# Kernel optimization log

Measured on AMD Instinct MI355X. Metric: run time of the kernel, lower is better.

## Reference

```python
import jax, jax.numpy as jnp
import numpy as np

B, T, C, H = 8, 1024, 768, 12
D = C // H  # head_dim = 64


def setup_inputs() -> dict:
    key = jax.random.key(0)
    ks = jax.random.split(key, 6)
    s = 1.0 / np.sqrt(C)
    x = jax.random.normal(ks[0], (B, T, C), dtype=jnp.float32)
    Wq = jax.random.normal(ks[1], (C, C), dtype=jnp.float32) * s
    Wk = jax.random.normal(ks[2], (C, C), dtype=jnp.float32) * s
    Wv = jax.random.normal(ks[3], (C, C), dtype=jnp.float32) * s
    Wo = jax.random.normal(ks[4], (C, C), dtype=jnp.float32) * s
    bq = jnp.zeros((C,), jnp.float32)
    bk = jnp.zeros((C,), jnp.float32)
    bv = jnp.zeros((C,), jnp.float32)
    bo = jnp.zeros((C,), jnp.float32)
    # causal mask, broadcastable to [B, H, T, T]
    mask = jnp.tril(jnp.ones((T, T), dtype=bool))[None, None, :, :]
    return {"x": x, "mask": mask, "Wq": Wq, "bq": bq, "Wk": Wk, "bk": bk,
            "Wv": Wv, "bv": bv, "Wo": Wo, "bo": bo}


def reference(x, mask, Wq, bq, Wk, bk, Wv, bv, Wo, bo):
    # QKV projections: [B,T,C] @ [C,C] -> [B,T,C]
    q = x @ Wq + bq
    k = x @ Wk + bk
    v = x @ Wv + bv
    # split heads -> [B,H,T,D]
    q = q.reshape(B, T, H, D).transpose(0, 2, 1, 3)
    k = k.reshape(B, T, H, D).transpose(0, 2, 1, 3)
    v = v.reshape(B, T, H, D).transpose(0, 2, 1, 3)
    scale = 1.0 / jnp.sqrt(jnp.float32(D))
    scores = jnp.einsum('bhtd,bhsd->bhts', q, k) * scale  # [B,H,T,T]
    scores = jnp.where(mask, scores, jnp.float32(-1e9))
    attn = jax.nn.softmax(scores, axis=-1)
    out = jnp.einsum('bhts,bhsd->bhtd', attn, v)  # [B,H,T,D]
    out = out.transpose(0, 2, 1, 3).reshape(B, T, C)
    return out @ Wo + bo
```

## Files before the change

### kernel.cpp

```cpp
#include <hip/hip_runtime.h>

#define B 8
#define T 1024
#define C 768
#define H 12
#define D 64
#define M (B * T)

typedef unsigned short u16;
typedef unsigned int u32;
typedef __attribute__((ext_vector_type(8))) short bf16x8;
typedef __attribute__((ext_vector_type(4))) float f32x4;

__device__ __forceinline__ u16 f2bf(float f) {
  union { float f; u32 u; } c; c.f = f;
  u32 r = c.u + 0x7FFF + ((c.u >> 16) & 1);
  return (u16)(r >> 16);
}

__device__ __forceinline__ void gload16(const void* g, void* l) {
  __builtin_amdgcn_global_load_lds(
      (const __attribute__((address_space(1))) void*)g,
      (__attribute__((address_space(3))) void*)l, 16, 0, 0);
}

__device__ __forceinline__ int swzA(int row) {
  return (row & 3) ^ ((row >> 2) & 1);
}

__global__ __launch_bounds__(256) void xconv_kernel(const float* __restrict__ in,
                                                    u16* __restrict__ out, int n4) {
  int i = blockIdx.x * 256 + threadIdx.x;
  int stride = gridDim.x * 256;
  for (; i < n4; i += stride) {
    float4 v = ((const float4*)in)[i];
    ushort4 o;
    o.x = f2bf(v.x); o.y = f2bf(v.y); o.z = f2bf(v.z); o.w = f2bf(v.w);
    ((ushort4*)out)[i] = o;
  }
}

__global__ __launch_bounds__(256) void wtrans_kernel(const float* __restrict__ Wq,
                                                     const float* __restrict__ Wk,
                                                     const float* __restrict__ Wv,
                                                     const float* __restrict__ Wo,
                                                     u16* __restrict__ WtQKV,
                                                     u16* __restrict__ WoT) {
  __shared__ float t[32][33];
  const int z = blockIdx.z;
  const float* W = (z == 0) ? Wq : (z == 1) ? Wk : (z == 2) ? Wv : Wo;
  u16* dst = (z < 3) ? (WtQKV + (size_t)z * 768 * 768) : WoT;
  const int k0 = blockIdx.y * 32, n0 = blockIdx.x * 32;
  const int tx = threadIdx.x & 31, ty = threadIdx.x >> 5;
#pragma unroll
  for (int i = 0; i < 4; i++) {
    int r = ty * 4 + i;
    t[r][tx] = W[(size_t)(k0 + r) * 768 + n0 + tx];
  }
  __syncthreads();
#pragma unroll
  for (int i = 0; i < 4; i++) {
    int r = ty * 4 + i;
    dst[(size_t)(n0 + r) * 768 + k0 + tx] = f2bf(t[tx][r]);
  }
}

template <typename OutT>
__global__ __launch_bounds__(256) void gemm_mfma_kernel(
    const u16* __restrict__ A,
    const u16* __restrict__ Wt,
    const float* __restrict__ b0, const float* __restrict__ b1, const float* __restrict__ b2,
    OutT* __restrict__ o0, OutT* __restrict__ o1, OutT* __restrict__ o2,
    float sc0, float sc1, float sc2) {
  __shared__ u16 As[128 * 32];
  __shared__ u16 Bs[128 * 32];
  const int tid = threadIdx.x;
  const int w = tid >> 6, l = tid & 63;
  const int g = l >> 4, c = l & 15;
  const int m0 = blockIdx.y * 128;
  const int n0g = blockIdx.x * 128;
  const int seg = n0g / 768;
  const int n0 = n0g - seg * 768;
  const float* bias = (seg == 0) ? b0 : (seg == 1) ? b1 : b2;
  OutT* out = (seg == 0) ? o0 : (seg == 1) ? o1 : o2;
  const float sc = (seg == 0) ? sc0 : (seg == 1) ? sc1 : sc2;
  const int wr = (w >> 1) * 64, wc = (w & 1) * 64;

  f32x4 acc[4][4];
#pragma unroll
  for (int i = 0; i < 4; i++)
#pragma unroll
    for (int j = 0; j < 4; j++) acc[i][j] = f32x4{0.f, 0.f, 0.f, 0.f};

  for (int k0 = 0; k0 < 768; k0 += 32) {
    __syncthreads();
#pragma unroll
    for (int t = 0; t < 2; t++) {
      int ii = w * 2 + t;
      int e16 = ii * 64 + l;
      int row = e16 >> 2, slot = e16 & 3;
      int gs = slot ^ swzA(row);
      gload16(A + (size_t)(m0 + row) * 768 + k0 + gs * 8, (char*)As + ii * 1024);
    }
#pragma unroll
    for (int t = 0; t < 2; t++) {
      int ii = w * 2 + t;
      int e16 = ii * 64 + l;
      int row = e16 >> 2, slot = e16 & 3;
      int gs = slot ^ swzA(row);
      gload16(Wt + (size_t)(n0g + row) * 768 + k0 + gs * 8, (char*)Bs + ii * 1024);
    }
    __syncthreads();

    bf16x8 af[4], bfr[4];
#pragma unroll
    for (int i = 0; i < 4; i++) {
      int row = wr + i * 16 + c;
      int slot = g ^ swzA(row);
      af[i] = *(const bf16x8*)(As + row * 32 + slot * 8);
    }
#pragma unroll
    for (int j = 0; j < 4; j++) {
      int row = wc + j * 16 + c;
      int slot = g ^ swzA(row);
      bfr[j] = *(const bf16x8*)(Bs + row * 32 + slot * 8);
    }
#pragma unroll
    for (int i = 0; i < 4; i++)
#pragma unroll
      for (int j = 0; j < 4; j++)
        acc[i][j] = __builtin_amdgcn_mfma_f32_16x16x32_bf16(af[i], bfr[j], acc[i][j], 0, 0, 0);
  }

#pragma unroll
  for (int j = 0; j < 4; j++) {
    int col = n0 + wc + j * 16 + c;
    float bb = bias[col];
#pragma unroll
    for (int i = 0; i < 4; i++) {
#pragma unroll
      for (int r = 0; r < 4; r++) {
        int row = m0 + wr + i * 16 + g * 4 + r;
        float v = (acc[i][j][r] + bb) * sc;
        if constexpr (sizeof(OutT) == 2) {
          ((u16*)out)[(size_t)row * 768 + col] = f2bf(v);
        } else {
          ((float*)out)[(size_t)row * 768 + col] = v;
        }
      }
    }
  }
}

__global__ __launch_bounds__(256) void attn_mfma_kernel(
    const u16* __restrict__ Qb, const u16* __restrict__ Kb,
    const u16* __restrict__ Vb, u16* __restrict__ Ob) {
  __shared__ u16 Ks[128 * 64];
  __shared__ u16 Vt[64][136];
  __shared__ u16 Ps[4][16][136];

  const int tid = threadIdx.x;
  const int w = tid >> 6, l = tid & 63;
  const int g = l >> 4, c = l & 15;

  const int wg = blockIdx.x;
  const int logical = (wg & 7) * 192 + (wg >> 3);
  const int bh = logical >> 4;
  const int qi = 15 - (logical & 15);
  const int q0 = qi * 64;
  const int b = bh / H, h = bh % H;
  const int qw = q0 + w * 16;

  bf16x8 qf[2];
  {
    size_t base = (size_t)(b * T + qw + c) * C + h * D;
    qf[0] = *(const bf16x8*)(Qb + base + g * 8);
    qf[1] = *(const bf16x8*)(Qb + base + 32 + g * 8);
  }

  f32x4 acc[4];
#pragma unroll
  for (int j = 0; j < 4; j++) acc[j] = f32x4{0.f, 0.f, 0.f, 0.f};
  float m_i[4], l_p[4];
#pragma unroll
  for (int r = 0; r < 4; r++) { m_i[r] = -1e30f; l_p[r] = 0.f; }

  const int nt = q0 / 128 + 1;
  for (int it = 0; it < nt; it++) {
    const int s0 = it * 128;
    __syncthreads();
#pragma unroll
    for (int t = 0; t < 4; t++) {
      int ii = w * 4 + t;
      int e16 = ii * 64 + l;
      int row = e16 >> 3, slot = e16 & 7;
      int gs = slot ^ (row & 7);
      gload16(Kb + (size_t)(b * T + s0 + row) * C + h * D + gs * 8, (char*)Ks + ii * 1024);
    }
    {
      int kv = tid & 127;
      int dh = tid >> 7;
      size_t vb = (size_t)(b * T + s0 + kv) * C + h * D + dh * 32;
#pragma unroll
      for (int rep = 0; rep < 4; rep++) {
        bf16x8 v8 = *(const bf16x8*)(Vb + vb + rep * 8);
        int d0 = dh * 32 + rep * 8;
#pragma unroll
        for (int e = 0; e < 8; e++) Vt[d0 + e][kv] = (u16)v8[e];
      }
    }
    __syncthreads();

    const bool active = (s0 <= qw + 15);
    if (active) {
      f32x4 s[8];
#pragma unroll
      for (int f = 0; f < 8; f++) s[f] = f32x4{0.f, 0.f, 0.f, 0.f};
#pragma unroll
      for (int f = 0; f < 8; f++) {
        int kvrow = f * 16 + c;
#pragma unroll
        for (int kc = 0; kc < 2; kc++) {
          int slot = (kc * 4 + g) ^ (kvrow & 7);
          bf16x8 kf = *(const bf16x8*)(Ks + kvrow * 64 + slot * 8);
          s[f] = __builtin_amdgcn_mfma_f32_16x16x32_bf16(qf[kc], kf, s[f], 0, 0, 0);
        }
      }
      const bool partial = (s0 + 127 > qw);
      if (partial) {
#pragma unroll
        for (int r = 0; r < 4; r++) {
          int q = qw + g * 4 + r;
#pragma unroll
          for (int f = 0; f < 8; f++) {
            int kv = s0 + f * 16 + c;
            if (kv > q) s[f][r] = -1e30f;
          }
        }
      }
      float mx[4];
#pragma unroll
      for (int r = 0; r < 4; r++) {
        float mr = s[0][r];
#pragma unroll
        for (int f = 1; f < 8; f++) mr = fmaxf(mr, s[f][r]);
        mx[r] = mr;
      }
#pragma unroll
      for (int off = 1; off < 16; off <<= 1)
#pragma unroll
        for (int r = 0; r < 4; r++) mx[r] = fmaxf(mx[r], __shfl_xor(mx[r], off, 64));
      bool defer = true;
#pragma unroll
      for (int r = 0; r < 4; r++) defer = defer && (mx[r] <= m_i[r] + 8.0f);
      if (!__all(defer)) {
#pragma unroll
        for (int r = 0; r < 4; r++) {
          float mn = fmaxf(m_i[r], mx[r]);
          float rc = exp2f(m_i[r] - mn);
          m_i[r] = mn;
          l_p[r] *= rc;
#pragma unroll
          for (int j = 0; j < 4; j++) acc[j][r] *= rc;
        }
      }
#pragma unroll
      for (int r = 0; r < 4; r++) {
        float sum = 0.f;
#pragma unroll
        for (int f = 0; f < 8; f++) {
          float p = exp2f(s[f][r] - m_i[r]);
          s[f][r] = p;
          sum += p;
        }
        l_p[r] += sum;
      }
#pragma unroll
      for (int f = 0; f < 8; f++)
#pragma unroll
        for (int r = 0; r < 4; r++)
          Ps[w][g * 4 + r][f * 16 + c] = f2bf(s[f][r]);
#pragma unroll
      for (int kc = 0; kc < 4; kc++) {
        bf16x8 pf = *(const bf16x8*)(&Ps[w][c][kc * 32 + g * 8]);
#pragma unroll
        for (int j = 0; j < 4; j++) {
          bf16x8 vf = *(const bf16x8*)(&Vt[j * 16 + c][kc * 32 + g * 8]);
          acc[j] = __builtin_amdgcn_mfma_f32_16x16x32_bf16(pf, vf, acc[j], 0, 0, 0);
        }
      }
    }
  }

  float inv[4];
#pragma unroll
  for (int r = 0; r < 4; r++) {
    float v = l_p[r];
#pragma unroll
    for (int off = 1; off < 16; off <<= 1) v += __shfl_xor(v, off, 64);
    inv[r] = 1.f / v;
  }
#pragma unroll
  for (int j = 0; j < 4; j++) {
#pragma unroll
    for (int r = 0; r < 4; r++) {
      int row = qw + g * 4 + r;
      int col = j * 16 + c;
      Ob[(size_t)(b * T + row) * C + h * D + col] = f2bf(acc[j][r] * inv[r]);
    }
  }
}

extern "C" void kernel_launch(void* const* d_in, const int* in_sizes, int n_in,
                              void* d_out, int out_size, void* d_ws, size_t ws_size,
                              hipStream_t stream) {
  const float* x  = (const float*)d_in[0];
  const float* Wq = (const float*)d_in[2];
  const float* bq = (const float*)d_in[3];
  const float* Wk = (const float*)d_in[4];
  const float* bk = (const float*)d_in[5];
  const float* Wv = (const float*)d_in[6];
  const float* bv = (const float*)d_in[7];
  const float* Wo = (const float*)d_in[8];
  const float* bo = (const float*)d_in[9];
  float* out = (float*)d_out;

  const size_t MC2 = (size_t)M * C * 2;
  char* ws = (char*)d_ws;
  u16* xb    = (u16*)(ws);
  u16* WtQKV = (u16*)(ws + MC2);
  u16* WoT   = (u16*)(ws + MC2 + 3538944);
  u16* Qb    = (u16*)(ws + MC2 + 3538944 + 1179648);
  u16* Kb    = (u16*)((char*)Qb + MC2);
  u16* Vb    = (u16*)((char*)Kb + MC2);
  u16* Ob    = (u16*)((char*)Vb + MC2);

  const float qscale = 0.125f * 1.4426950408889634f;

  xconv_kernel<<<2048, 256, 0, stream>>>(x, xb, M * C / 4);
  wtrans_kernel<<<dim3(24, 24, 4), 256, 0, stream>>>(Wq, Wk, Wv, Wo, WtQKV, WoT);
  gemm_mfma_kernel<u16><<<dim3(18, 64), 256, 0, stream>>>(
      xb, WtQKV, bq, bk, bv, Qb, Kb, Vb, qscale, 1.f, 1.f);
  attn_mfma_kernel<<<1536, 256, 0, stream>>>(Qb, Kb, Vb, Ob);
  gemm_mfma_kernel<float><<<dim3(6, 64), 256, 0, stream>>>(
      Ob, WoT, bo, bo, bo, out, out, out, 1.f, 1.f, 1.f);
}
```

Measured before the change: 144.7 us.

## Produce V transposed via swapped GEMM and load it with async LDS copies

The V projection is now computed as Wv^T·x^T in its own GEMM launch, giving a [C, M] transposed V with row-wise bias. The attention kernel can then stream V tiles straight into swizzled shared memory with global_load_lds instead of doing a per-element register transpose into LDS. The P tile padding shrinks and P is converted to bf16 two values at a time with the packed intrinsic. This removes scalar LDS transpose stores in the attention loop at the cost of an extra GEMM launch. The VT output writes in that GEMM stride by M, so they may be less coalesced.

```diff
diff --git a/kernel.cpp b/kernel.cpp
--- a/kernel.cpp
+++ b/kernel.cpp
@@ -1,4 +1,5 @@
 #include <hip/hip_runtime.h>
+#include <hip/hip_bf16.h>
 
 #define B 8
 #define T 1024
@@ -65,13 +66,13 @@
   }
 }
 
-template <typename OutT>
+template <typename OutT, bool ROWBIAS>
 __global__ __launch_bounds__(256) void gemm_mfma_kernel(
     const u16* __restrict__ A,
     const u16* __restrict__ Wt,
-    const float* __restrict__ b0, const float* __restrict__ b1, const float* __restrict__ b2,
-    OutT* __restrict__ o0, OutT* __restrict__ o1, OutT* __restrict__ o2,
-    float sc0, float sc1, float sc2) {
+    const float* __restrict__ b0, const float* __restrict__ b1,
+    OutT* __restrict__ o0, OutT* __restrict__ o1,
+    int ldOut, float sc0, float sc1) {
   __shared__ u16 As[128 * 32];
   __shared__ u16 Bs[128 * 32];
   const int tid = threadIdx.x;
@@ -79,11 +80,11 @@
   const int g = l >> 4, c = l & 15;
   const int m0 = blockIdx.y * 128;
   const int n0g = blockIdx.x * 128;
-  const int seg = n0g / 768;
+  const int seg = (!ROWBIAS && n0g >= 768) ? 1 : 0;
   const int n0 = n0g - seg * 768;
-  const float* bias = (seg == 0) ? b0 : (seg == 1) ? b1 : b2;
-  OutT* out = (seg == 0) ? o0 : (seg == 1) ? o1 : o2;
-  const float sc = (seg == 0) ? sc0 : (seg == 1) ? sc1 : sc2;
+  const float* bias = (seg == 0) ? b0 : b1;
+  OutT* out = (seg == 0) ? o0 : o1;
+  const float sc = (seg == 0) ? sc0 : sc1;
   const int wr = (w >> 1) * 64, wc = (w & 1) * 64;
 
   f32x4 acc[4][4];
@@ -132,20 +133,28 @@
         acc[i][j] = __builtin_amdgcn_mfma_f32_16x16x32_bf16(af[i], bfr[j], acc[i][j], 0, 0, 0);
   }
 
+  float brow[4][4];
+  if (ROWBIAS) {
+#pragma unroll
+    for (int i = 0; i < 4; i++)
+#pragma unroll
+      for (int r = 0; r < 4; r++)
+        brow[i][r] = b0[m0 + wr + i * 16 + g * 4 + r];
+  }
 #pragma unroll
   for (int j = 0; j < 4; j++) {
     int col = n0 + wc + j * 16 + c;
-    float bb = bias[col];
+    float bcol = ROWBIAS ? 0.f : bias[col];
 #pragma unroll
     for (int i = 0; i < 4; i++) {
 #pragma unroll
       for (int r = 0; r < 4; r++) {
         int row = m0 + wr + i * 16 + g * 4 + r;
-        float v = (acc[i][j][r] + bb) * sc;
+        float v = (acc[i][j][r] + (ROWBIAS ? brow[i][r] : bcol)) * sc;
         if constexpr (sizeof(OutT) == 2) {
-          ((u16*)out)[(size_t)row * 768 + col] = f2bf(v);
+          ((u16*)out)[(size_t)row * ldOut + col] = f2bf(v);
         } else {
-          ((float*)out)[(size_t)row * 768 + col] = v;
+          ((float*)out)[(size_t)row * ldOut + col] = v;
         }
       }
     }
@@ -154,10 +163,10 @@
 
 __global__ __launch_bounds__(256) void attn_mfma_kernel(
     const u16* __restrict__ Qb, const u16* __restrict__ Kb,
-    const u16* __restrict__ Vb, u16* __restrict__ Ob) {
+    const u16* __restrict__ VT, u16* __restrict__ Ob) {
   __shared__ u16 Ks[128 * 64];
-  __shared__ u16 Vt[64][136];
-  __shared__ u16 Ps[4][16][136];
+  __shared__ u16 Vs[64 * 128];
+  __shared__ u16 Ps[4][16][132];
 
   const int tid = threadIdx.x;
   const int w = tid >> 6, l = tid & 63;
@@ -197,17 +206,13 @@
       int gs = slot ^ (row & 7);
       gload16(Kb + (size_t)(b * T + s0 + row) * C + h * D + gs * 8, (char*)Ks + ii * 1024);
     }
-    {
-      int kv = tid & 127;
-      int dh = tid >> 7;
-      size_t vb = (size_t)(b * T + s0 + kv) * C + h * D + dh * 32;
-#pragma unroll
-      for (int rep = 0; rep < 4; rep++) {
-        bf16x8 v8 = *(const bf16x8*)(Vb + vb + rep * 8);
-        int d0 = dh * 32 + rep * 8;
-#pragma unroll
-        for (int e = 0; e < 8; e++) Vt[d0 + e][kv] = (u16)v8[e];
-      }
+#pragma unroll
+    for (int t = 0; t < 4; t++) {
+      int ii = w * 4 + t;
+      int e16 = ii * 64 + l;
+      int row = e16 >> 4, slot = e16 & 15;
+      int gs = slot ^ (row & 15);
+      gload16(VT + (size_t)(h * D + row) * M + b * T + s0 + gs * 8, (char*)Vs + ii * 1024);
     }
     __syncthreads();
 
@@ -274,18 +279,20 @@
           sum += p;
         }
         l_p[r] += sum;
-      }
-#pragma unroll
-      for (int f = 0; f < 8; f++)
-#pragma unroll
-        for (int r = 0; r < 4; r++)
-          Ps[w][g * 4 + r][f * 16 + c] = f2bf(s[f][r]);
+#pragma unroll
+        for (int f = 0; f < 8; f += 2) {
+          __hip_bfloat162 h2 = __float22bfloat162_rn(make_float2(s[f][r], s[f + 1][r]));
+          u32 pk = *(u32*)&h2;
+          Ps[w][g * 4 + r][f * 16 + c] = (u16)pk;
+          Ps[w][g * 4 + r][(f + 1) * 16 + c] = (u16)(pk >> 16);
+        }
+      }
 #pragma unroll
       for (int kc = 0; kc < 4; kc++) {
         bf16x8 pf = *(const bf16x8*)(&Ps[w][c][kc * 32 + g * 8]);
 #pragma unroll
         for (int j = 0; j < 4; j++) {
-          bf16x8 vf = *(const bf16x8*)(&Vt[j * 16 + c][kc * 32 + g * 8]);
+          bf16x8 vf = *(const bf16x8*)(Vs + (j * 16 + c) * 128 + (((kc * 4 + g) ^ c) * 8));
           acc[j] = __builtin_amdgcn_mfma_f32_16x16x32_bf16(pf, vf, acc[j], 0, 0, 0);
         }
       }
@@ -332,16 +339,19 @@
   u16* WoT   = (u16*)(ws + MC2 + 3538944);
   u16* Qb    = (u16*)(ws + MC2 + 3538944 + 1179648);
   u16* Kb    = (u16*)((char*)Qb + MC2);
-  u16* Vb    = (u16*)((char*)Kb + MC2);
-  u16* Ob    = (u16*)((char*)Vb + MC2);
+  u16* VT    = (u16*)((char*)Kb + MC2);
+  u16* Ob    = (u16*)((char*)VT + MC2);
+  u16* WvT   = WtQKV + 2 * 768 * 768;
 
   const float qscale = 0.125f * 1.4426950408889634f;
 
   xconv_kernel<<<2048, 256, 0, stream>>>(x, xb, M * C / 4);
   wtrans_kernel<<<dim3(24, 24, 4), 256, 0, stream>>>(Wq, Wk, Wv, Wo, WtQKV, WoT);
-  gemm_mfma_kernel<u16><<<dim3(18, 64), 256, 0, stream>>>(
-      xb, WtQKV, bq, bk, bv, Qb, Kb, Vb, qscale, 1.f, 1.f);
-  attn_mfma_kernel<<<1536, 256, 0, stream>>>(Qb, Kb, Vb, Ob);
-  gemm_mfma_kernel<float><<<dim3(6, 64), 256, 0, stream>>>(
-      Ob, WoT, bo, bo, bo, out, out, out, 1.f, 1.f, 1.f);
-}
+  gemm_mfma_kernel<u16, false><<<dim3(12, 64), 256, 0, stream>>>(
+      xb, WtQKV, bq, bk, Qb, Kb, 768, qscale, 1.f);
+  gemm_mfma_kernel<u16, true><<<dim3(64, 6), 256, 0, stream>>>(
+      WvT, xb, bv, bv, VT, VT, M, 1.f, 1.f);
+  attn_mfma_kernel<<<1536, 256, 0, stream>>>(Qb, Kb, VT, Ob);
+  gemm_mfma_kernel<float, false><<<dim3(6, 64), 256, 0, stream>>>(
+      Ob, WoT, bo, bo, out, out, 768, 1.f, 1.f);
+}
```

Measured after the change: 139.3 us. 1.04x faster.
